# Kernel tuning notes

Measured on AMD Instinct MI355X. Metric: run time of the kernel, lower is better.

## Reference

```python
import jax, jax.numpy as jnp
import numpy as np

N_NODES = 100000
D_SRC = 128
D_DST = 128
D_OUT = 256
N_EDGES = 600000


def setup_inputs() -> dict:
    key = jax.random.key(0)
    k1, k2, k3, k4, k5 = jax.random.split(key, 5)
    x_src = jax.random.normal(k1, (N_NODES, D_SRC), dtype=jnp.float32)
    x_dst = jax.random.normal(k2, (N_NODES, D_DST), dtype=jnp.float32)
    edge_index = jax.random.randint(k3, (2, N_EDGES), 0, N_NODES, dtype=jnp.int64)
    # Linear(in_src + in_dst, out): torch stores W as [out, in]
    fan_in = D_SRC + D_DST
    bound = 1.0 / np.sqrt(fan_in)
    W = jax.random.uniform(k4, (D_OUT, fan_in), minval=-bound, maxval=bound, dtype=jnp.float32)
    b = jax.random.uniform(k5, (D_OUT,), minval=-bound, maxval=bound, dtype=jnp.float32)
    return {"x_src": x_src, "x_dst": x_dst, "edge_index": edge_index, "W": W, "b": b}


def reference(x_src, x_dst, edge_index, W, b):
    src_idx, dst_idx = edge_index[0], edge_index[1]
    n_dst = x_dst.shape[0]
    x_j = x_src[src_idx]                                  # [E, D_SRC] gather
    summed = jax.ops.segment_sum(x_j, dst_idx, num_segments=n_dst)   # [N, D_SRC]
    count = jax.ops.segment_sum(jnp.ones((src_idx.shape[0],), dtype=x_src.dtype),
                                dst_idx, num_segments=n_dst)          # [N]
    agg = summed / jnp.maximum(count, 1.0)[:, None]        # scatter-mean
    h = jnp.concatenate([x_dst, agg], axis=-1)             # [N, D_DST+D_SRC]
    return jax.nn.relu(h @ W.T + b)                        # [N, D_OUT]
```

## Files before the change

### kernel.cpp

```cpp
#include <hip/hip_runtime.h>

#define N_NODES 100000
#define D_SRC 128
#define D_OUT 256
#define K_DIM 256
#define CAP 32
#define OVF_CAP 2048

typedef __attribute__((ext_vector_type(8))) short short8;
typedef __attribute__((ext_vector_type(4))) float float4v;
typedef __attribute__((ext_vector_type(4))) unsigned int uint4v;

__device__ inline unsigned short f2bf(float f) {
    unsigned int u = __float_as_uint(f);
    u += 0x7FFF + ((u >> 16) & 1);
    return (unsigned short)(u >> 16);
}
__device__ inline float bf_lo(unsigned int u) { return __uint_as_float(u << 16); }
__device__ inline float bf_hi(unsigned int u) { return __uint_as_float(u & 0xFFFF0000u); }

#define PREP_SRC_BLOCKS 12500
#define PREP_DST_BLOCKS 6250
#define PREP_W_BLOCKS   32

__global__ __launch_bounds__(256) void prep_kernel(
    const float* __restrict__ x_src,
    const float* __restrict__ x_dst,
    const float* __restrict__ W,
    const int*   __restrict__ ei,
    unsigned short* __restrict__ xsb,
    unsigned short* __restrict__ xdsw,
    unsigned short* __restrict__ wsw,
    int* __restrict__ deg,
    int* __restrict__ ovf_cnt,
    int* __restrict__ ovf,
    int* __restrict__ bucket,
    int n_edges, int nb_bucket)
{
    int b = blockIdx.x;
    if (b < nb_bucket) {
        int e = b * 256 + threadIdx.x;
        if (e < n_edges) {
            int s = ei[e];
            int d = ei[n_edges + e];
            int pos = atomicAdd(deg + d, 1);
            if (pos < CAP) {
                bucket[(size_t)d * CAP + pos] = s;
            } else {
                int o = atomicAdd(ovf_cnt, 1);
                if (o < OVF_CAP) { ovf[2 * o] = s; ovf[2 * o + 1] = d; }
            }
        }
        return;
    }
    b -= nb_bucket;
    if (b < PREP_SRC_BLOCKS) {
        int i = b * 256 + threadIdx.x;
        float4 v = ((const float4*)x_src)[i];
        ushort4 o;
        o.x = f2bf(v.x); o.y = f2bf(v.y); o.z = f2bf(v.z); o.w = f2bf(v.w);
        ((ushort4*)xsb)[i] = o;
    } else if (b < PREP_SRC_BLOCKS + PREP_DST_BLOCKS) {
        int t = (b - PREP_SRC_BLOCKS) * 256 + threadIdx.x;
        int r = t >> 4;
        int g = t & 15;
        const float4* p = (const float4*)(x_dst + (size_t)r * 128 + g * 8);
        float4 v0 = p[0], v1 = p[1];
        union { unsigned short s[8]; short8 v; } pk;
        pk.s[0] = f2bf(v0.x); pk.s[1] = f2bf(v0.y);
        pk.s[2] = f2bf(v0.z); pk.s[3] = f2bf(v0.w);
        pk.s[4] = f2bf(v1.x); pk.s[5] = f2bf(v1.y);
        pk.s[6] = f2bf(v1.z); pk.s[7] = f2bf(v1.w);
        size_t gr = ((size_t)(r >> 4) * 4 + (g >> 2)) * 64 + (r & 15) + ((g & 3) << 4);
        ((short8*)xdsw)[gr] = pk.v;
    } else {
        int t = (b - PREP_SRC_BLOCKS - PREP_DST_BLOCKS) * 256 + threadIdx.x;
        int r = t >> 5;
        int g = t & 31;
        const float4* p = (const float4*)(W + (size_t)r * 256 + g * 8);
        float4 v0 = p[0], v1 = p[1];
        union { unsigned short s[8]; short8 v; } pk;
        pk.s[0] = f2bf(v0.x); pk.s[1] = f2bf(v0.y);
        pk.s[2] = f2bf(v0.z); pk.s[3] = f2bf(v0.w);
        pk.s[4] = f2bf(v1.x); pk.s[5] = f2bf(v1.y);
        pk.s[6] = f2bf(v1.z); pk.s[7] = f2bf(v1.w);
        size_t gr = ((size_t)(r >> 4) * 8 + (g >> 2)) * 64 + (r & 15) + ((g & 3) << 4);
        ((short8*)wsw)[gr] = pk.v;
    }
}

#define G_ISSUE8(U, V, B, I0, I1, I2, I3, N0, N1, N2, N3)                     \
    {                                                                         \
        int r_ = (B) + grp;                                                   \
        { bool v_ = r_ < N0; V[0] = v_; int s_ = __shfl(I0, r_);              \
          s_ = v_ ? s_ : 0;                                                   \
          U[0] = *(const uint4v*)(xsb + (size_t)s_ * D_SRC + gcol * 8); }     \
        { bool v_ = r_ < N1; V[1] = v_; int s_ = __shfl(I1, r_);              \
          s_ = v_ ? s_ : 0;                                                   \
          U[1] = *(const uint4v*)(xsb + (size_t)s_ * D_SRC + gcol * 8); }     \
        { bool v_ = r_ < N2; V[2] = v_; int s_ = __shfl(I2, r_);              \
          s_ = v_ ? s_ : 0;                                                   \
          U[2] = *(const uint4v*)(xsb + (size_t)s_ * D_SRC + gcol * 8); }     \
        { bool v_ = r_ < N3; V[3] = v_; int s_ = __shfl(I3, r_);              \
          s_ = v_ ? s_ : 0;                                                   \
          U[3] = *(const uint4v*)(xsb + (size_t)s_ * D_SRC + gcol * 8); }     \
    }

#define G_ACC1(ACC, W)                                                       \
    ACC[0] += bf_lo(W[0]); ACC[1] += bf_hi(W[0]);                            \
    ACC[2] += bf_lo(W[1]); ACC[3] += bf_hi(W[1]);                            \
    ACC[4] += bf_lo(W[2]); ACC[5] += bf_hi(W[2]);                            \
    ACC[6] += bf_lo(W[3]); ACC[7] += bf_hi(W[3]);

#define G_ACCUM8(U, V, A0, A1, A2, A3)                                       \
    if (V[0]) { G_ACC1(A0, U[0]) }                                           \
    if (V[1]) { G_ACC1(A1, U[1]) }                                           \
    if (V[2]) { G_ACC1(A2, U[2]) }                                           \
    if (V[3]) { G_ACC1(A3, U[3]) }

__global__ __launch_bounds__(256) void gather_kernel(
    const unsigned short* __restrict__ xsb,
    const int*   __restrict__ deg,
    const int*   __restrict__ bucket,
    const int*   __restrict__ ovf_cnt,
    const int*   __restrict__ ovf,
    unsigned int* __restrict__ aggsw)
{
    int wid  = threadIdx.x >> 6;
    int lane = threadIdx.x & 63;
    int wbase = (blockIdx.x * 4 + wid) * 8;
    int grp  = lane >> 4;
    int gcol = lane & 15;

    int dl = deg[wbase + (lane & 7)];
    int dtA0 = __shfl(dl, 0), dtA1 = __shfl(dl, 1);
    int dtA2 = __shfl(dl, 2), dtA3 = __shfl(dl, 3);
    int dtB0 = __shfl(dl, 4), dtB1 = __shfl(dl, 5);
    int dtB2 = __shfl(dl, 6), dtB3 = __shfl(dl, 7);
    int nA0 = min(dtA0, CAP), nA1 = min(dtA1, CAP);
    int nA2 = min(dtA2, CAP), nA3 = min(dtA3, CAP);
    int nB0 = min(dtB0, CAP), nB1 = min(dtB1, CAP);
    int nB2 = min(dtB2, CAP), nB3 = min(dtB3, CAP);

    int iA0 = bucket[(size_t)(wbase + 0) * CAP + (lane & 31)];
    int iA1 = bucket[(size_t)(wbase + 1) * CAP + (lane & 31)];
    int iA2 = bucket[(size_t)(wbase + 2) * CAP + (lane & 31)];
    int iA3 = bucket[(size_t)(wbase + 3) * CAP + (lane & 31)];
    int iB0 = bucket[(size_t)(wbase + 4) * CAP + (lane & 31)];
    int iB1 = bucket[(size_t)(wbase + 5) * CAP + (lane & 31)];
    int iB2 = bucket[(size_t)(wbase + 6) * CAP + (lane & 31)];
    int iB3 = bucket[(size_t)(wbase + 7) * CAP + (lane & 31)];

    float accA0[8] = {0,0,0,0,0,0,0,0}, accA1[8] = {0,0,0,0,0,0,0,0};
    float accA2[8] = {0,0,0,0,0,0,0,0}, accA3[8] = {0,0,0,0,0,0,0,0};
    float accB0[8] = {0,0,0,0,0,0,0,0}, accB1[8] = {0,0,0,0,0,0,0,0};
    float accB2[8] = {0,0,0,0,0,0,0,0}, accB3[8] = {0,0,0,0,0,0,0,0};

    int maxn = max(max(max(nA0, nA1), max(nA2, nA3)),
                   max(max(nB0, nB1), max(nB2, nB3)));

    uint4v uAa[4], uAb[4], uBa[4], uBb[4];
    bool   vAa[4], vAb[4], vBa[4], vBb[4];
    if (maxn > 0) {
        G_ISSUE8(uAa, vAa, 0, iA0, iA1, iA2, iA3, nA0, nA1, nA2, nA3)
        G_ISSUE8(uBa, vBa, 0, iB0, iB1, iB2, iB3, nB0, nB1, nB2, nB3)
        int bb = 0;
        while (true) {
            if (bb + 4 < maxn) {
                G_ISSUE8(uAb, vAb, bb + 4, iA0, iA1, iA2, iA3, nA0, nA1, nA2, nA3)
                G_ISSUE8(uBb, vBb, bb + 4, iB0, iB1, iB2, iB3, nB0, nB1, nB2, nB3)
            }
            G_ACCUM8(uAa, vAa, accA0, accA1, accA2, accA3)
            G_ACCUM8(uBa, vBa, accB0, accB1, accB2, accB3)
            bb += 4;
            if (bb >= maxn) break;
            if (bb + 4 < maxn) {
                G_ISSUE8(uAa, vAa, bb + 4, iA0, iA1, iA2, iA3, nA0, nA1, nA2, nA3)
                G_ISSUE8(uBa, vBa, bb + 4, iB0, iB1, iB2, iB3, nB0, nB1, nB2, nB3)
            }
            G_ACCUM8(uAb, vAb, accA0, accA1, accA2, accA3)
            G_ACCUM8(uBb, vBb, accB0, accB1, accB2, accB3)
            bb += 4;
            if (bb >= maxn) break;
        }
    }

    if ((dtA0 > CAP) | (dtA1 > CAP) | (dtA2 > CAP) | (dtA3 > CAP) |
        (dtB0 > CAP) | (dtB1 > CAP) | (dtB2 > CAP) | (dtB3 > CAP)) {
        int oc = *ovf_cnt;
        if (oc > OVF_CAP) oc = OVF_CAP;
        for (int o = 0; o < oc; ++o) {
            int od  = ovf[2 * o + 1];
            int rel = od - wbase;
            if (rel >= 0 && rel < 8) {
                int s0 = ovf[2 * o];
                uint4v w = *(const uint4v*)(xsb + (size_t)s0 * D_SRC + gcol * 8);
                if (grp == 0) {
                    if      (rel == 0) { G_ACC1(accA0, w) }
                    else if (rel == 1) { G_ACC1(accA1, w) }
                    else if (rel == 2) { G_ACC1(accA2, w) }
                    else if (rel == 3) { G_ACC1(accA3, w) }
                    else if (rel == 4) { G_ACC1(accB0, w) }
                    else if (rel == 5) { G_ACC1(accB1, w) }
                    else if (rel == 6) { G_ACC1(accB2, w) }
                    else               { G_ACC1(accB3, w) }
                }
            }
        }
    }

    #pragma unroll
    for (int k = 0; k < 8; ++k) {
        accA0[k] += __shfl_xor(accA0[k], 16); accA0[k] += __shfl_xor(accA0[k], 32);
        accA1[k] += __shfl_xor(accA1[k], 16); accA1[k] += __shfl_xor(accA1[k], 32);
        accA2[k] += __shfl_xor(accA2[k], 16); accA2[k] += __shfl_xor(accA2[k], 32);
        accA3[k] += __shfl_xor(accA3[k], 16); accA3[k] += __shfl_xor(accA3[k], 32);
        accB0[k] += __shfl_xor(accB0[k], 16); accB0[k] += __shfl_xor(accB0[k], 32);
        accB1[k] += __shfl_xor(accB1[k], 16); accB1[k] += __shfl_xor(accB1[k], 32);
        accB2[k] += __shfl_xor(accB2[k], 16); accB2[k] += __shfl_xor(accB2[k], 32);
        accB3[k] += __shfl_xor(accB3[k], 16); accB3[k] += __shfl_xor(accB3[k], 32);
    }

    {
        int dsel = dtA0;
        dsel = (grp == 1) ? dtA1 : dsel;
        dsel = (grp == 2) ? dtA2 : dsel;
        dsel = (grp == 3) ? dtA3 : dsel;
        float inv = 1.0f / (float)((dsel > 1) ? dsel : 1);
        float sum[8];
        #pragma unroll
        for (int k = 0; k < 8; ++k) {
            float v = accA0[k];
            v = (grp == 1) ? accA1[k] : v;
            v = (grp == 2) ? accA2[k] : v;
            v = (grp == 3) ? accA3[k] : v;
            sum[k] = v * inv;
        }
        uint4v o;
        o[0] = (unsigned)f2bf(sum[0]) | ((unsigned)f2bf(sum[1]) << 16);
        o[1] = (unsigned)f2bf(sum[2]) | ((unsigned)f2bf(sum[3]) << 16);
        o[2] = (unsigned)f2bf(sum[4]) | ((unsigned)f2bf(sum[5]) << 16);
        o[3] = (unsigned)f2bf(sum[6]) | ((unsigned)f2bf(sum[7]) << 16);
        int node = wbase + grp;
        size_t gr = ((size_t)(node >> 4) * 4 + (gcol >> 2)) * 64
                  + (node & 15) + ((gcol & 3) << 4);
        ((uint4v*)aggsw)[gr] = o;
    }
    {
        int dsel = dtB0;
        dsel = (grp == 1) ? dtB1 : dsel;
        dsel = (grp == 2) ? dtB2 : dsel;
        dsel = (grp == 3) ? dtB3 : dsel;
        float inv = 1.0f / (float)((dsel > 1) ? dsel : 1);
        float sum[8];
        #pragma unroll
        for (int k = 0; k < 8; ++k) {
            float v = accB0[k];
            v = (grp == 1) ? accB1[k] : v;
            v = (grp == 2) ? accB2[k] : v;
            v = (grp == 3) ? accB3[k] : v;
            sum[k] = v * inv;
        }
        uint4v o;
        o[0] = (unsigned)f2bf(sum[0]) | ((unsigned)f2bf(sum[1]) << 16);
        o[1] = (unsigned)f2bf(sum[2]) | ((unsigned)f2bf(sum[3]) << 16);
        o[2] = (unsigned)f2bf(sum[4]) | ((unsigned)f2bf(sum[5]) << 16);
        o[3] = (unsigned)f2bf(sum[6]) | ((unsigned)f2bf(sum[7]) << 16);
        int node = wbase + 4 + grp;
        size_t gr = ((size_t)(node >> 4) * 4 + (gcol >> 2)) * 64
                  + (node & 15) + ((gcol & 3) << 4);
        ((uint4v*)aggsw)[gr] = o;
    }
}

__global__ __launch_bounds__(256) void mfma_gemm_kernel(
    const short8* __restrict__ xdsw,
    const short8* __restrict__ aggsw,
    const short8* __restrict__ wsw,
    const float* __restrict__ bias,
    float*       __restrict__ out)
{
    __shared__ float eps[4][16][68];

    int wave = threadIdx.x >> 6;
    int lane = threadIdx.x & 63;
    int lrow = lane & 15;
    int kq   = lane >> 4;
    int mb   = blockIdx.x;
    int m0   = mb * 64;
    int n0   = wave * 64;

    bool mok[4];
    #pragma unroll
    for (int mf = 0; mf < 4; ++mf) mok[mf] = (m0 + mf * 16) < N_NODES;

    const short8* Ax = xdsw  + (size_t)mb * 1024 + lane;
    const short8* Ag = aggsw + (size_t)mb * 1024 + lane;
    const short8* Bw = wsw   + (size_t)wave * 2048 + lane;

    float4v acc[4][4];
    #pragma unroll
    for (int i = 0; i < 4; ++i)
        #pragma unroll
        for (int j = 0; j < 4; ++j)
            acc[i][j] = (float4v){0.f, 0.f, 0.f, 0.f};

    const short8 zfrag = (short8){0,0,0,0,0,0,0,0};
    short8 a[2][4], b[2][4];

    #pragma unroll
    for (int mf = 0; mf < 4; ++mf)
        a[0][mf] = mok[mf] ? Ax[mf * 256] : zfrag;
    #pragma unroll
    for (int nf = 0; nf < 4; ++nf)
        b[0][nf] = Bw[nf * 512];

    #pragma unroll
    for (int kc = 0; kc < 8; ++kc) {
        const int cur = kc & 1, nxt = cur ^ 1;
        if (kc < 7) {
            const int k1 = kc + 1;
            const short8* A = (k1 < 4) ? Ax : Ag;
            const int kk = (k1 < 4) ? k1 : (k1 - 4);
            #pragma unroll
            for (int mf = 0; mf < 4; ++mf)
                a[nxt][mf] = mok[mf] ? A[mf * 256 + kk * 64] : zfrag;
            #pragma unroll
            for (int nf = 0; nf < 4; ++nf)
                b[nxt][nf] = Bw[nf * 512 + k1 * 64];
        }
        #pragma unroll
        for (int mf = 0; mf < 4; ++mf)
            #pragma unroll
            for (int nf = 0; nf < 4; ++nf)
                acc[mf][nf] = __builtin_amdgcn_mfma_f32_16x16x32_bf16(
                    a[cur][mf], b[cur][nf], acc[mf][nf], 0, 0, 0);
    }

    float bv[4];
    #pragma unroll
    for (int nf = 0; nf < 4; ++nf)
        bv[nf] = bias[n0 + nf * 16 + lrow];

    int srow   = lane >> 4;
    int schunk = lane & 15;

    #pragma unroll
    for (int mf = 0; mf < 4; ++mf) {
        if (!mok[mf]) continue;
        #pragma unroll
        for (int nf = 0; nf < 4; ++nf)
            #pragma unroll
            for (int r = 0; r < 4; ++r)
                eps[wave][kq * 4 + r][nf * 16 + lrow] =
                    fmaxf(acc[mf][nf][r] + bv[nf], 0.f);
        asm volatile("s_waitcnt lgkmcnt(0)" ::: "memory");
        #pragma unroll
        for (int c = 0; c < 4; ++c) {
            int row  = c * 4 + srow;
            float4v v = *(const float4v*)&eps[wave][row][schunk * 4];
            int grow = m0 + mf * 16 + row;
            __builtin_nontemporal_store(v,
                (float4v*)(out + (size_t)grow * D_OUT + n0 + schunk * 4));
        }
        asm volatile("s_waitcnt lgkmcnt(0)" ::: "memory");
    }
}

extern "C" void kernel_launch(void* const* d_in, const int* in_sizes, int n_in,
                              void* d_out, int out_size, void* d_ws, size_t ws_size,
                              hipStream_t stream) {
    const float* x_src = (const float*)d_in[0];
    const float* x_dst = (const float*)d_in[1];
    const int*   ei    = (const int*)d_in[2];
    const float* W     = (const float*)d_in[3];
    const float* bias  = (const float*)d_in[4];
    float* out = (float*)d_out;

    int n_edges = in_sizes[2] / 2;

    int* deg     = (int*)d_ws;
    int* ovf_cnt = deg + N_NODES;
    int* ovf     = ovf_cnt + 4;
    unsigned short* wsw   = (unsigned short*)(ovf + OVF_CAP * 2);
    unsigned short* aggsw = wsw + (size_t)D_OUT * K_DIM;
    unsigned short* xdsw  = aggsw + (size_t)(N_NODES / 16) * 4 * 64 * 8;

    int* bucket = (int*)d_out;
    unsigned short* xsb = (unsigned short*)(bucket + (size_t)N_NODES * CAP);

    hipMemsetAsync(d_ws, 0, (N_NODES + 4) * sizeof(int), stream);

    int nb_bucket = (n_edges + 255) / 256;
    int prep_blocks = nb_bucket + PREP_SRC_BLOCKS + PREP_DST_BLOCKS + PREP_W_BLOCKS;
    prep_kernel<<<prep_blocks, 256, 0, stream>>>(
        x_src, x_dst, W, ei, xsb, xdsw, wsw,
        deg, ovf_cnt, ovf, bucket, n_edges, nb_bucket);

    gather_kernel<<<(N_NODES + 31) / 32, 256, 0, stream>>>(
        xsb, deg, bucket, ovf_cnt, ovf, (unsigned int*)aggsw);

    mfma_gemm_kernel<<<(N_NODES + 63) / 64, 256, 0, stream>>>(
        (const short8*)xdsw, (const short8*)aggsw, (const short8*)wsw, bias, out);
}
```

Baseline: 287.9 us.

## Store per-node degree in bucket row header and move dst/W packing into gather kernel

The per-node edge counter moves into slot 0 of each 32-int bucket row, leaving 31 source slots. The gather kernel then reads the count from the same row load it already issues for indices, removing the separate deg array and its dependent load. The x_dst and W bf16 packing moves from the first prep kernel into the gather kernel's grid, so that packing can overlap with the memory-bound gather. In exchange, the whole bucket array (about 12.8 MB) must now be zeroed with a memset instead of a small degree array, and each row holds one fewer inline slot before edges spill to the overflow list.

```diff
diff --git a/kernel.cpp b/kernel.cpp
--- a/kernel.cpp
+++ b/kernel.cpp
@@ -4,7 +4,8 @@
 #define D_SRC 128
 #define D_OUT 256
 #define K_DIM 256
-#define CAP 32
+#define ROW 32
+#define SLOTS 31
 #define OVF_CAP 2048
 
 typedef __attribute__((ext_vector_type(8))) short short8;
@@ -20,21 +21,14 @@
 __device__ inline float bf_hi(unsigned int u) { return __uint_as_float(u & 0xFFFF0000u); }
 
 #define PREP_SRC_BLOCKS 12500
-#define PREP_DST_BLOCKS 6250
-#define PREP_W_BLOCKS   32
-
-__global__ __launch_bounds__(256) void prep_kernel(
+
+__global__ __launch_bounds__(256) void k_bucket_src(
+    const int*   __restrict__ ei,
     const float* __restrict__ x_src,
-    const float* __restrict__ x_dst,
-    const float* __restrict__ W,
-    const int*   __restrict__ ei,
-    unsigned short* __restrict__ xsb,
-    unsigned short* __restrict__ xdsw,
-    unsigned short* __restrict__ wsw,
-    int* __restrict__ deg,
+    int* __restrict__ bucket,
     int* __restrict__ ovf_cnt,
     int* __restrict__ ovf,
-    int* __restrict__ bucket,
+    unsigned short* __restrict__ xsb,
     int n_edges, int nb_bucket)
 {
     int b = blockIdx.x;
@@ -43,9 +37,9 @@
         if (e < n_edges) {
             int s = ei[e];
             int d = ei[n_edges + e];
-            int pos = atomicAdd(deg + d, 1);
-            if (pos < CAP) {
-                bucket[(size_t)d * CAP + pos] = s;
+            int pos = atomicAdd(bucket + (size_t)d * ROW, 1);
+            if (pos < SLOTS) {
+                bucket[(size_t)d * ROW + 1 + pos] = s;
             } else {
                 int o = atomicAdd(ovf_cnt, 1);
                 if (o < OVF_CAP) { ovf[2 * o] = s; ovf[2 * o + 1] = d; }
@@ -53,55 +47,26 @@
         }
         return;
     }
-    b -= nb_bucket;
-    if (b < PREP_SRC_BLOCKS) {
-        int i = b * 256 + threadIdx.x;
-        float4 v = ((const float4*)x_src)[i];
-        ushort4 o;
-        o.x = f2bf(v.x); o.y = f2bf(v.y); o.z = f2bf(v.z); o.w = f2bf(v.w);
-        ((ushort4*)xsb)[i] = o;
-    } else if (b < PREP_SRC_BLOCKS + PREP_DST_BLOCKS) {
-        int t = (b - PREP_SRC_BLOCKS) * 256 + threadIdx.x;
-        int r = t >> 4;
-        int g = t & 15;
-        const float4* p = (const float4*)(x_dst + (size_t)r * 128 + g * 8);
-        float4 v0 = p[0], v1 = p[1];
-        union { unsigned short s[8]; short8 v; } pk;
-        pk.s[0] = f2bf(v0.x); pk.s[1] = f2bf(v0.y);
-        pk.s[2] = f2bf(v0.z); pk.s[3] = f2bf(v0.w);
-        pk.s[4] = f2bf(v1.x); pk.s[5] = f2bf(v1.y);
-        pk.s[6] = f2bf(v1.z); pk.s[7] = f2bf(v1.w);
-        size_t gr = ((size_t)(r >> 4) * 4 + (g >> 2)) * 64 + (r & 15) + ((g & 3) << 4);
-        ((short8*)xdsw)[gr] = pk.v;
-    } else {
-        int t = (b - PREP_SRC_BLOCKS - PREP_DST_BLOCKS) * 256 + threadIdx.x;
-        int r = t >> 5;
-        int g = t & 31;
-        const float4* p = (const float4*)(W + (size_t)r * 256 + g * 8);
-        float4 v0 = p[0], v1 = p[1];
-        union { unsigned short s[8]; short8 v; } pk;
-        pk.s[0] = f2bf(v0.x); pk.s[1] = f2bf(v0.y);
-        pk.s[2] = f2bf(v0.z); pk.s[3] = f2bf(v0.w);
-        pk.s[4] = f2bf(v1.x); pk.s[5] = f2bf(v1.y);
-        pk.s[6] = f2bf(v1.z); pk.s[7] = f2bf(v1.w);
-        size_t gr = ((size_t)(r >> 4) * 8 + (g >> 2)) * 64 + (r & 15) + ((g & 3) << 4);
-        ((short8*)wsw)[gr] = pk.v;
-    }
+    int i = (b - nb_bucket) * 256 + threadIdx.x;
+    float4 v = ((const float4*)x_src)[i];
+    ushort4 o;
+    o.x = f2bf(v.x); o.y = f2bf(v.y); o.z = f2bf(v.z); o.w = f2bf(v.w);
+    ((ushort4*)xsb)[i] = o;
 }
 
 #define G_ISSUE8(U, V, B, I0, I1, I2, I3, N0, N1, N2, N3)                     \
     {                                                                         \
         int r_ = (B) + grp;                                                   \
-        { bool v_ = r_ < N0; V[0] = v_; int s_ = __shfl(I0, r_);              \
+        { bool v_ = r_ < N0; V[0] = v_; int s_ = __shfl(I0, 1 + r_);          \
           s_ = v_ ? s_ : 0;                                                   \
           U[0] = *(const uint4v*)(xsb + (size_t)s_ * D_SRC + gcol * 8); }     \
-        { bool v_ = r_ < N1; V[1] = v_; int s_ = __shfl(I1, r_);              \
+        { bool v_ = r_ < N1; V[1] = v_; int s_ = __shfl(I1, 1 + r_);          \
           s_ = v_ ? s_ : 0;                                                   \
           U[1] = *(const uint4v*)(xsb + (size_t)s_ * D_SRC + gcol * 8); }     \
-        { bool v_ = r_ < N2; V[2] = v_; int s_ = __shfl(I2, r_);              \
+        { bool v_ = r_ < N2; V[2] = v_; int s_ = __shfl(I2, 1 + r_);          \
           s_ = v_ ? s_ : 0;                                                   \
           U[2] = *(const uint4v*)(xsb + (size_t)s_ * D_SRC + gcol * 8); }     \
-        { bool v_ = r_ < N3; V[3] = v_; int s_ = __shfl(I3, r_);              \
+        { bool v_ = r_ < N3; V[3] = v_; int s_ = __shfl(I3, 1 + r_);          \
           s_ = v_ ? s_ : 0;                                                   \
           U[3] = *(const uint4v*)(xsb + (size_t)s_ * D_SRC + gcol * 8); }     \
     }
@@ -118,38 +83,77 @@
     if (V[2]) { G_ACC1(A2, U[2]) }                                           \
     if (V[3]) { G_ACC1(A3, U[3]) }
 
-__global__ __launch_bounds__(256) void gather_kernel(
+#define GATHER_BLOCKS 3125
+#define PREP_DST_BLOCKS 6250
+#define PREP_W_BLOCKS   32
+
+__global__ __launch_bounds__(256) void k_gather_pack(
     const unsigned short* __restrict__ xsb,
-    const int*   __restrict__ deg,
     const int*   __restrict__ bucket,
     const int*   __restrict__ ovf_cnt,
     const int*   __restrict__ ovf,
-    unsigned int* __restrict__ aggsw)
+    unsigned int* __restrict__ aggsw,
+    const float* __restrict__ x_dst,
+    const float* __restrict__ W,
+    unsigned short* __restrict__ xdsw,
+    unsigned short* __restrict__ wsw)
 {
+    int blk = blockIdx.x;
+    if (blk >= GATHER_BLOCKS) {
+        int pb = blk - GATHER_BLOCKS;
+        if (pb < PREP_DST_BLOCKS) {
+            int t = pb * 256 + threadIdx.x;
+            int r = t >> 4;
+            int g = t & 15;
+            const float4* p = (const float4*)(x_dst + (size_t)r * 128 + g * 8);
+            float4 v0 = p[0], v1 = p[1];
+            union { unsigned short s[8]; short8 v; } pk;
+            pk.s[0] = f2bf(v0.x); pk.s[1] = f2bf(v0.y);
+            pk.s[2] = f2bf(v0.z); pk.s[3] = f2bf(v0.w);
+            pk.s[4] = f2bf(v1.x); pk.s[5] = f2bf(v1.y);
+            pk.s[6] = f2bf(v1.z); pk.s[7] = f2bf(v1.w);
+            size_t gr = ((size_t)(r >> 4) * 4 + (g >> 2)) * 64 + (r & 15) + ((g & 3) << 4);
+            ((short8*)xdsw)[gr] = pk.v;
+        } else {
+            int t = (pb - PREP_DST_BLOCKS) * 256 + threadIdx.x;
+            int r = t >> 5;
+            int g = t & 31;
+            const float4* p = (const float4*)(W + (size_t)r * 256 + g * 8);
+            float4 v0 = p[0], v1 = p[1];
+            union { unsigned short s[8]; short8 v; } pk;
+            pk.s[0] = f2bf(v0.x); pk.s[1] = f2bf(v0.y);
+            pk.s[2] = f2bf(v0.z); pk.s[3] = f2bf(v0.w);
+            pk.s[4] = f2bf(v1.x); pk.s[5] = f2bf(v1.y);
+            pk.s[6] = f2bf(v1.z); pk.s[7] = f2bf(v1.w);
+            size_t gr = ((size_t)(r >> 4) * 8 + (g >> 2)) * 64 + (r & 15) + ((g & 3) << 4);
+            ((short8*)wsw)[gr] = pk.v;
+        }
+        return;
+    }
+
     int wid  = threadIdx.x >> 6;
     int lane = threadIdx.x & 63;
-    int wbase = (blockIdx.x * 4 + wid) * 8;
+    int wbase = (blk * 4 + wid) * 8;
     int grp  = lane >> 4;
     int gcol = lane & 15;
 
-    int dl = deg[wbase + (lane & 7)];
-    int dtA0 = __shfl(dl, 0), dtA1 = __shfl(dl, 1);
-    int dtA2 = __shfl(dl, 2), dtA3 = __shfl(dl, 3);
-    int dtB0 = __shfl(dl, 4), dtB1 = __shfl(dl, 5);
-    int dtB2 = __shfl(dl, 6), dtB3 = __shfl(dl, 7);
-    int nA0 = min(dtA0, CAP), nA1 = min(dtA1, CAP);
-    int nA2 = min(dtA2, CAP), nA3 = min(dtA3, CAP);
-    int nB0 = min(dtB0, CAP), nB1 = min(dtB1, CAP);
-    int nB2 = min(dtB2, CAP), nB3 = min(dtB3, CAP);
-
-    int iA0 = bucket[(size_t)(wbase + 0) * CAP + (lane & 31)];
-    int iA1 = bucket[(size_t)(wbase + 1) * CAP + (lane & 31)];
-    int iA2 = bucket[(size_t)(wbase + 2) * CAP + (lane & 31)];
-    int iA3 = bucket[(size_t)(wbase + 3) * CAP + (lane & 31)];
-    int iB0 = bucket[(size_t)(wbase + 4) * CAP + (lane & 31)];
-    int iB1 = bucket[(size_t)(wbase + 5) * CAP + (lane & 31)];
-    int iB2 = bucket[(size_t)(wbase + 6) * CAP + (lane & 31)];
-    int iB3 = bucket[(size_t)(wbase + 7) * CAP + (lane & 31)];
+    int iA0 = bucket[(size_t)(wbase + 0) * ROW + (lane & 31)];
+    int iA1 = bucket[(size_t)(wbase + 1) * ROW + (lane & 31)];
+    int iA2 = bucket[(size_t)(wbase + 2) * ROW + (lane & 31)];
+    int iA3 = bucket[(size_t)(wbase + 3) * ROW + (lane & 31)];
+    int iB0 = bucket[(size_t)(wbase + 4) * ROW + (lane & 31)];
+    int iB1 = bucket[(size_t)(wbase + 5) * ROW + (lane & 31)];
+    int iB2 = bucket[(size_t)(wbase + 6) * ROW + (lane & 31)];
+    int iB3 = bucket[(size_t)(wbase + 7) * ROW + (lane & 31)];
+
+    int dtA0 = __shfl(iA0, 0), dtA1 = __shfl(iA1, 0);
+    int dtA2 = __shfl(iA2, 0), dtA3 = __shfl(iA3, 0);
+    int dtB0 = __shfl(iB0, 0), dtB1 = __shfl(iB1, 0);
+    int dtB2 = __shfl(iB2, 0), dtB3 = __shfl(iB3, 0);
+    int nA0 = min(dtA0, SLOTS), nA1 = min(dtA1, SLOTS);
+    int nA2 = min(dtA2, SLOTS), nA3 = min(dtA3, SLOTS);
+    int nB0 = min(dtB0, SLOTS), nB1 = min(dtB1, SLOTS);
+    int nB2 = min(dtB2, SLOTS), nB3 = min(dtB3, SLOTS);
 
     float accA0[8] = {0,0,0,0,0,0,0,0}, accA1[8] = {0,0,0,0,0,0,0,0};
     float accA2[8] = {0,0,0,0,0,0,0,0}, accA3[8] = {0,0,0,0,0,0,0,0};
@@ -185,8 +189,8 @@
         }
     }
 
-    if ((dtA0 > CAP) | (dtA1 > CAP) | (dtA2 > CAP) | (dtA3 > CAP) |
-        (dtB0 > CAP) | (dtB1 > CAP) | (dtB2 > CAP) | (dtB3 > CAP)) {
+    if ((dtA0 > SLOTS) | (dtA1 > SLOTS) | (dtA2 > SLOTS) | (dtA3 > SLOTS) |
+        (dtB0 > SLOTS) | (dtB1 > SLOTS) | (dtB2 > SLOTS) | (dtB3 > SLOTS)) {
         int oc = *ovf_cnt;
         if (oc > OVF_CAP) oc = OVF_CAP;
         for (int o = 0; o < oc; ++o) {
@@ -379,26 +383,24 @@
 
     int n_edges = in_sizes[2] / 2;
 
-    int* deg     = (int*)d_ws;
-    int* ovf_cnt = deg + N_NODES;
+    int* ovf_cnt = (int*)d_ws;
     int* ovf     = ovf_cnt + 4;
     unsigned short* wsw   = (unsigned short*)(ovf + OVF_CAP * 2);
     unsigned short* aggsw = wsw + (size_t)D_OUT * K_DIM;
     unsigned short* xdsw  = aggsw + (size_t)(N_NODES / 16) * 4 * 64 * 8;
 
     int* bucket = (int*)d_out;
-    unsigned short* xsb = (unsigned short*)(bucket + (size_t)N_NODES * CAP);
-
-    hipMemsetAsync(d_ws, 0, (N_NODES + 4) * sizeof(int), stream);
+    unsigned short* xsb = (unsigned short*)(bucket + (size_t)N_NODES * ROW);
+
+    hipMemsetAsync(ovf_cnt, 0, 16, stream);
+    hipMemsetAsync(bucket, 0, (size_t)N_NODES * ROW * sizeof(int), stream);
 
     int nb_bucket = (n_edges + 255) / 256;
-    int prep_blocks = nb_bucket + PREP_SRC_BLOCKS + PREP_DST_BLOCKS + PREP_W_BLOCKS;
-    prep_kernel<<<prep_blocks, 256, 0, stream>>>(
-        x_src, x_dst, W, ei, xsb, xdsw, wsw,
-        deg, ovf_cnt, ovf, bucket, n_edges, nb_bucket);
-
-    gather_kernel<<<(N_NODES + 31) / 32, 256, 0, stream>>>(
-        xsb, deg, bucket, ovf_cnt, ovf, (unsigned int*)aggsw);
+    k_bucket_src<<<nb_bucket + PREP_SRC_BLOCKS, 256, 0, stream>>>(
+        ei, x_src, bucket, ovf_cnt, ovf, xsb, n_edges, nb_bucket);
+
+    k_gather_pack<<<GATHER_BLOCKS + PREP_DST_BLOCKS + PREP_W_BLOCKS, 256, 0, stream>>>(
+        xsb, bucket, ovf_cnt, ovf, (unsigned int*)aggsw, x_dst, W, xdsw, wsw);
 
     mfma_gemm_kernel<<<(N_NODES + 63) / 64, 256, 0, stream>>>(
         (const short8*)xdsw, (const short8*)aggsw, (const short8*)wsw, bias, out);
```

Measured after the change: 276.9 us. 1.04x faster.
